# Performance work log

Measured on AMD Instinct MI355X. Metric: run time of the kernel, lower is better.

The kernel has to match this reference:

```python
import jax, jax.numpy as jnp
import numpy as np

INTERP = 10  # gt contour interpolation factor (time=10 in source)
SMOOTH_L1_BETA = 1.0
LOSS_WEIGHT = 1.0


def interpolation(poly):
    # poly: [B, M, 2] -> [B, M*INTERP, 2]
    poly_roll = jnp.roll(poly, shift=1, axis=1)
    step = jnp.arange(INTERP, dtype=poly.dtype) / INTERP  # [INTERP]
    # [B, M, INTERP, 2]
    interp = (poly[:, :, None, :] * step[None, None, :, None]
              + poly_roll[:, :, None, :] * (1.0 - step)[None, None, :, None])
    B, M = poly.shape[0], poly.shape[1]
    return interp.reshape(B, M * INTERP, 2)


def compute_distance(pred, gt):
    # pred: [B, N, 2], gt: [B, M, 2] -> squared euclidean distance [B, M, N]
    # ||g - p||^2 = ||g||^2 + ||p||^2 - 2 g.p  (avoids materializing [B,M,N,2])
    g2 = jnp.sum(gt * gt, axis=-1)[:, :, None]    # [B, M, 1]
    p2 = jnp.sum(pred * pred, axis=-1)[:, None, :]  # [B, 1, N]
    gp = jnp.einsum('bmk,bnk->bmn', gt, pred)
    return g2 + p2 - 2.0 * gp


def smooth_l1(x, y):
    d = jnp.abs(x - y)
    return jnp.where(d < SMOOTH_L1_BETA, 0.5 * d * d / SMOOTH_L1_BETA, d - 0.5 * SMOOTH_L1_BETA)


def setup_inputs() -> dict:
    key = jax.random.key(0)
    k1, k2, k3, k4 = jax.random.split(key, 4)
    B, N, M = 1024, 128, 128
    ini_pred_poly = jax.random.normal(k1, (B, N, 2), dtype=jnp.float32)
    pred_poly = ini_pred_poly + 0.1 * jax.random.normal(k2, (B, N, 2), dtype=jnp.float32)
    gt_poly = jax.random.normal(k3, (B, M, 2), dtype=jnp.float32)
    keyPointsMask = (jax.random.uniform(k4, (B, M)) < 0.7).astype(jnp.float32)
    return {'ini_pred_poly': ini_pred_poly, 'pred_poly': pred_poly,
            'gt_poly': gt_poly, 'keyPointsMask': keyPointsMask}


def reference(ini_pred_poly, pred_poly, gt_poly, keyPointsMask):
    # --- lossPred2NearestGt ---
    gt_interp = interpolation(gt_poly)                       # [B, M*10, 2]
    d1 = compute_distance(ini_pred_poly, gt_interp)          # [B, M*10, N]
    index_gt = jnp.argmin(d1, axis=1)                        # [B, N]
    nearest_gt = jnp.take_along_axis(gt_interp, index_gt[:, :, None], axis=1)  # [B, N, 2]
    loss_pred2gt = jnp.mean(smooth_l1(pred_poly, nearest_gt))  # scalar (reduction='mean')

    # --- lossGt2NearestPred ---
    d2 = compute_distance(ini_pred_poly, gt_poly)            # [B, M, N]
    index_pred = jnp.argmin(d2, axis=2)                      # [B, M]
    nearest_pred = jnp.take_along_axis(pred_poly, index_pred[:, :, None], axis=1)  # [B, M, 2]
    loss_gt2pred = smooth_l1(nearest_pred, gt_poly)          # [B, M, 2] (reduction='none')

    # mask expanded to [B, M, 2] in the source -> its sum counts both coords
    mask = keyPointsMask[:, :, None]
    masked_sum = jnp.sum(loss_gt2pred * mask)
    mask_sum = 2.0 * jnp.sum(keyPointsMask)
    loss_set2set = masked_sum / (mask_sum + 1.0) + loss_pred2gt
    loss = loss_set2set / 2.0
    return LOSS_WEIGHT * loss
```

## Files before the change

kernel.cpp:

```cpp
#include <hip/hip_runtime.h>
#include <math.h>


#define BB 1024
#define NN 128
#define MM 128

__device__ __forceinline__ float sl1(float x) {
    float d = fabsf(x);
    return d < 1.0f ? 0.5f * d * d : d - 0.5f;
}

__global__ void __launch_bounds__(512, 4)
dmloss_main(const float* __restrict__ ini, const float* __restrict__ pred,
            const float* __restrict__ gt,  const float* __restrict__ kmask,
            float4* __restrict__ partials)
{
    const int b   = blockIdx.x;
    const int tid = threadIdx.x;
    const int g   = tid & 63;
    const int h   = tid >> 6;

    __shared__ __align__(16) float2 s_gt[MM];
    __shared__ float2 s_pr[NN];
    __shared__ float2 s_ii[NN];
    __shared__ float4 s_segA[MM];
    __shared__ float2 s_segB[MM];
    __shared__ float  s_step[16];
    __shared__ float  s_rv[8 * 128];
    __shared__ float  s_rf[8 * 128];
    __shared__ float  s_sum[3][8];

    const float2* gt2 = (const float2*)(gt   + (size_t)b * MM * 2);
    const float2* in2 = (const float2*)(ini  + (size_t)b * NN * 2);
    const float2* pr2 = (const float2*)(pred + (size_t)b * NN * 2);

    float2 myPr = make_float2(0.f, 0.f);
    float  myKm = 0.f;
    if (tid < 128) {
        int m = tid;
        float2 gm = gt2[m];
        float2 a  = gt2[(m + 127) & 127];
        s_gt[m] = gm;
        float ex = gm.x - a.x, ey = gm.y - a.y;
        float A  = ex * ex + ey * ey;
        float inv = A > 0.f ? 10.f / A : 0.f;
        s_segA[m] = make_float4(a.x, a.y, -ex * inv, -ey * inv);
        s_segB[m] = make_float2(ex * 0.1f, ey * 0.1f);
        myPr = pr2[m];
        myKm = kmask[b * MM + m];
    } else if (tid < 256) {
        s_pr[tid - 128] = pr2[tid - 128];
    } else if (tid < 384) {
        s_ii[tid - 256] = in2[tid - 256];
    } else if (tid < 400) {
        s_step[tid - 384] = (float)(tid - 384) / 10.0f;
    }

    float4 pv = *(const float4*)(&in2[2 * g]);
    const float px0 = pv.x, py0 = pv.y, px1 = pv.z, py1 = pv.w;
    __syncthreads();

    float sumA = 0.f, sumB = 0.f, sumC = 0.f;

    float b0 = INFINITY, b1 = INFINITY;
    float f0 = 1e30f, f1 = 1e30f;
    {
        float fm = (float)(160 * h);
        const int m0 = 16 * h;
        #pragma unroll 2
        for (int j = 0; j < 16; ++j) {
            float4 SA = s_segA[m0 + j];
            float2 SB = s_segB[m0 + j];
            const float ax = SA.x, ay = SA.y, Xn = SA.z, Yn = SA.w;
            const float ux = SB.x, uy = SB.y;
            {
                float qx = ax - px0, qy = ay - py0;
                float jv = fmaf(qy, Yn, qx * Xn);
                float jr = rintf(__builtin_amdgcn_fmed3f(jv, 0.f, 9.f));
                float dx = fmaf(jr, ux, qx);
                float dy = fmaf(jr, uy, qy);
                float d  = fmaf(dy, dy, dx * dx);
                float fi = fm + jr;
                if (d < b0) { b0 = d; f0 = fi; }
            }
            {
                float qx = ax - px1, qy = ay - py1;
                float jv = fmaf(qy, Yn, qx * Xn);
                float jr = rintf(__builtin_amdgcn_fmed3f(jv, 0.f, 9.f));
                float dx = fmaf(jr, ux, qx);
                float dy = fmaf(jr, uy, qy);
                float d  = fmaf(dy, dy, dx * dx);
                float fi = fm + jr;
                if (d < b1) { b1 = d; f1 = fi; }
            }
            fm += 10.f;
        }
    }
    {
        float2* rv2 = (float2*)&s_rv[h * 128 + 2 * g];
        float2* rf2 = (float2*)&s_rf[h * 128 + 2 * g];
        *rv2 = make_float2(b0, b1);
        *rf2 = make_float2(f0, f1);
    }
    __syncthreads();

    if (tid < 128) {
        float best = s_rv[tid], bf = s_rf[tid];
        #pragma unroll
        for (int q = 1; q < 8; ++q) {
            float ov = s_rv[q * 128 + tid];
            float of = s_rf[q * 128 + tid];
            if (ov < best || (ov == best && of < bf)) { best = ov; bf = of; }
        }
        int bidx = (int)bf;
        int m = bidx / 10;
        int j = bidx - m * 10;
        float s  = s_step[j];
        float tt = 1.0f - s;
        float2 gm = s_gt[m];
        float2 gp = s_gt[(m + 127) & 127];
        float gx = gm.x * s + gp.x * tt;
        float gy = gm.y * s + gp.y * tt;
        sumA = sl1(myPr.x - gx) + sl1(myPr.y - gy);
    }
    __syncthreads();

    {
        float4 gv = *(const float4*)(&s_gt[2 * g]);
        const float gx0 = gv.x, gy0 = gv.y, gx1 = gv.z, gy1 = gv.w;
        b0 = INFINITY; b1 = INFINITY;
        f0 = 1e30f; f1 = 1e30f;
        float fk = (float)(16 * h);
        const int k0 = 16 * h;
        #pragma unroll 4
        for (int j = 0; j < 16; ++j) {
            float2 I = s_ii[k0 + j];
            {
                float dx = I.x - gx0, dy = I.y - gy0;
                float d  = fmaf(dy, dy, dx * dx);
                if (d < b0) { b0 = d; f0 = fk; }
            }
            {
                float dx = I.x - gx1, dy = I.y - gy1;
                float d  = fmaf(dy, dy, dx * dx);
                if (d < b1) { b1 = d; f1 = fk; }
            }
            fk += 1.f;
        }
        float2* rv2 = (float2*)&s_rv[h * 128 + 2 * g];
        float2* rf2 = (float2*)&s_rf[h * 128 + 2 * g];
        *rv2 = make_float2(b0, b1);
        *rf2 = make_float2(f0, f1);
    }
    __syncthreads();

    if (tid < 128) {
        float best = s_rv[tid], bf = s_rf[tid];
        #pragma unroll
        for (int q = 1; q < 8; ++q) {
            float ov = s_rv[q * 128 + tid];
            float of = s_rf[q * 128 + tid];
            if (ov < best || (ov == best && of < bf)) { best = ov; bf = of; }
        }
        int k = (int)bf;
        float2 pk2 = s_pr[k];
        float2 g0  = s_gt[tid];
        sumB = myKm * (sl1(pk2.x - g0.x) + sl1(pk2.y - g0.y));
        sumC = myKm;
    }

    #pragma unroll
    for (int off = 32; off > 0; off >>= 1) {
        sumA += __shfl_down(sumA, off);
        sumB += __shfl_down(sumB, off);
        sumC += __shfl_down(sumC, off);
    }
    const int wave = tid >> 6;
    if ((tid & 63) == 0) {
        s_sum[0][wave] = sumA; s_sum[1][wave] = sumB; s_sum[2][wave] = sumC;
    }
    __syncthreads();
    if (tid == 0) {
        float A = 0.f, Bs = 0.f, C = 0.f;
        #pragma unroll
        for (int w = 0; w < 8; ++w) {
            A += s_sum[0][w]; Bs += s_sum[1][w]; C += s_sum[2][w];
        }
        partials[b] = make_float4(A, Bs, C, 0.0f);
    }
}

__global__ void __launch_bounds__(256)
dmloss_final(const float4* __restrict__ partials, float* __restrict__ out)
{
    const int tid = threadIdx.x;
    float A = 0.0f, Bs = 0.0f, C = 0.0f;
    #pragma unroll
    for (int i = tid; i < BB; i += 256) {
        float4 p = partials[i];
        A += p.x; Bs += p.y; C += p.z;
    }
    #pragma unroll
    for (int off = 32; off > 0; off >>= 1) {
        A  += __shfl_down(A, off);
        Bs += __shfl_down(Bs, off);
        C  += __shfl_down(C, off);
    }
    __shared__ float sA[4], sB[4], sC[4];
    const int wave = tid >> 6, lane = tid & 63;
    if (lane == 0) { sA[wave] = A; sB[wave] = Bs; sC[wave] = C; }
    __syncthreads();
    if (tid == 0) {
        float a  = sA[0] + sA[1] + sA[2] + sA[3];
        float bs = sB[0] + sB[1] + sB[2] + sB[3];
        float c  = sC[0] + sC[1] + sC[2] + sC[3];
        float loss_pred2gt = a / ((float)BB * (float)NN * 2.0f);
        float loss_set2set = bs / (2.0f * c + 1.0f) + loss_pred2gt;
        out[0] = 0.5f * loss_set2set;
    }
}

extern "C" void kernel_launch(void* const* d_in, const int* in_sizes, int n_in,
                              void* d_out, int out_size, void* d_ws, size_t ws_size,
                              hipStream_t stream)
{
    const float* ini   = (const float*)d_in[0];
    const float* pred  = (const float*)d_in[1];
    const float* gt    = (const float*)d_in[2];
    const float* kmask = (const float*)d_in[3];
    float4* partials = (float4*)d_ws;

    dmloss_main<<<dim3(BB), dim3(512), 0, stream>>>(ini, pred, gt, kmask, partials);
    dmloss_final<<<dim3(1), dim3(256), 0, stream>>>(partials, (float*)d_out);
}
```

Before: 19.08 us.

## Split pred2gt and gt2pred phases into separate blocks per batch

Measured after the change: 20.33 us. 1.07x slower.

```diff
diff --git a/kernel.cpp b/kernel.cpp
--- a/kernel.cpp
+++ b/kernel.cpp
@@ -12,21 +12,22 @@
 }
 
 __global__ void __launch_bounds__(512, 4)
-dmloss_main(const float* __restrict__ ini, const float* __restrict__ pred,
-            const float* __restrict__ gt,  const float* __restrict__ kmask,
-            float4* __restrict__ partials)
+dmloss_phase(const float* __restrict__ ini, const float* __restrict__ pred,
+             const float* __restrict__ gt,  const float* __restrict__ kmask,
+             float* __restrict__ pA, float2* __restrict__ pBC)
 {
-    const int b   = blockIdx.x;
+    const int bid = blockIdx.x;
+    const int b   = bid >> 1;
     const int tid = threadIdx.x;
     const int g   = tid & 63;
     const int h   = tid >> 6;
 
     __shared__ __align__(16) float2 s_gt[MM];
-    __shared__ float2 s_pr[NN];
-    __shared__ float2 s_ii[NN];
     __shared__ float4 s_segA[MM];
     __shared__ float2 s_segB[MM];
     __shared__ float  s_step[16];
+    __shared__ float2 s_pr[NN];
+    __shared__ float2 s_ii[NN];
     __shared__ float  s_rv[8 * 128];
     __shared__ float  s_rf[8 * 128];
     __shared__ float  s_sum[3][8];
@@ -34,172 +35,174 @@
     const float2* gt2 = (const float2*)(gt   + (size_t)b * MM * 2);
     const float2* in2 = (const float2*)(ini  + (size_t)b * NN * 2);
     const float2* pr2 = (const float2*)(pred + (size_t)b * NN * 2);
-
-    float2 myPr = make_float2(0.f, 0.f);
-    float  myKm = 0.f;
-    if (tid < 128) {
-        int m = tid;
-        float2 gm = gt2[m];
-        float2 a  = gt2[(m + 127) & 127];
-        s_gt[m] = gm;
-        float ex = gm.x - a.x, ey = gm.y - a.y;
-        float A  = ex * ex + ey * ey;
-        float inv = A > 0.f ? 10.f / A : 0.f;
-        s_segA[m] = make_float4(a.x, a.y, -ex * inv, -ey * inv);
-        s_segB[m] = make_float2(ex * 0.1f, ey * 0.1f);
-        myPr = pr2[m];
-        myKm = kmask[b * MM + m];
-    } else if (tid < 256) {
-        s_pr[tid - 128] = pr2[tid - 128];
-    } else if (tid < 384) {
-        s_ii[tid - 256] = in2[tid - 256];
-    } else if (tid < 400) {
-        s_step[tid - 384] = (float)(tid - 384) / 10.0f;
-    }
-
-    float4 pv = *(const float4*)(&in2[2 * g]);
-    const float px0 = pv.x, py0 = pv.y, px1 = pv.z, py1 = pv.w;
-    __syncthreads();
-
-    float sumA = 0.f, sumB = 0.f, sumC = 0.f;
-
-    float b0 = INFINITY, b1 = INFINITY;
-    float f0 = 1e30f, f1 = 1e30f;
-    {
-        float fm = (float)(160 * h);
-        const int m0 = 16 * h;
-        #pragma unroll 2
-        for (int j = 0; j < 16; ++j) {
-            float4 SA = s_segA[m0 + j];
-            float2 SB = s_segB[m0 + j];
-            const float ax = SA.x, ay = SA.y, Xn = SA.z, Yn = SA.w;
-            const float ux = SB.x, uy = SB.y;
-            {
-                float qx = ax - px0, qy = ay - py0;
-                float jv = fmaf(qy, Yn, qx * Xn);
-                float jr = rintf(__builtin_amdgcn_fmed3f(jv, 0.f, 9.f));
-                float dx = fmaf(jr, ux, qx);
-                float dy = fmaf(jr, uy, qy);
-                float d  = fmaf(dy, dy, dx * dx);
-                float fi = fm + jr;
-                if (d < b0) { b0 = d; f0 = fi; }
-            }
-            {
-                float qx = ax - px1, qy = ay - py1;
-                float jv = fmaf(qy, Yn, qx * Xn);
-                float jr = rintf(__builtin_amdgcn_fmed3f(jv, 0.f, 9.f));
-                float dx = fmaf(jr, ux, qx);
-                float dy = fmaf(jr, uy, qy);
-                float d  = fmaf(dy, dy, dx * dx);
-                float fi = fm + jr;
-                if (d < b1) { b1 = d; f1 = fi; }
-            }
-            fm += 10.f;
-        }
-    }
-    {
-        float2* rv2 = (float2*)&s_rv[h * 128 + 2 * g];
-        float2* rf2 = (float2*)&s_rf[h * 128 + 2 * g];
-        *rv2 = make_float2(b0, b1);
-        *rf2 = make_float2(f0, f1);
-    }
-    __syncthreads();
-
-    if (tid < 128) {
-        float best = s_rv[tid], bf = s_rf[tid];
+    const int wave = tid >> 6;
+
+    if ((bid & 1) == 0) {
+        float2 myPr = make_float2(0.f, 0.f);
+        if (tid < 128) {
+            int m = tid;
+            float2 gm = gt2[m];
+            float2 a  = gt2[(m + 127) & 127];
+            s_gt[m] = gm;
+            float ex = gm.x - a.x, ey = gm.y - a.y;
+            float A  = ex * ex + ey * ey;
+            float inv = A > 0.f ? 10.f / A : 0.f;
+            s_segA[m] = make_float4(a.x, a.y, -ex * inv, -ey * inv);
+            s_segB[m] = make_float2(ex * 0.1f, ey * 0.1f);
+            myPr = pr2[m];
+        } else if (tid < 144) {
+            s_step[tid - 128] = (float)(tid - 128) / 10.0f;
+        }
+        float4 pv = *(const float4*)(&in2[2 * g]);
+        const float px0 = pv.x, py0 = pv.y, px1 = pv.z, py1 = pv.w;
+        __syncthreads();
+
+        float b0 = INFINITY, b1 = INFINITY;
+        float f0 = 1e30f, f1 = 1e30f;
+        {
+            float fm = (float)(160 * h);
+            const int m0 = 16 * h;
+            #pragma unroll 2
+            for (int j = 0; j < 16; ++j) {
+                float4 SA = s_segA[m0 + j];
+                float2 SB = s_segB[m0 + j];
+                const float ax = SA.x, ay = SA.y, Xn = SA.z, Yn = SA.w;
+                const float ux = SB.x, uy = SB.y;
+                {
+                    float qx = ax - px0, qy = ay - py0;
+                    float jv = fmaf(qy, Yn, qx * Xn);
+                    float jr = rintf(__builtin_amdgcn_fmed3f(jv, 0.f, 9.f));
+                    float dx = fmaf(jr, ux, qx);
+                    float dy = fmaf(jr, uy, qy);
+                    float d  = fmaf(dy, dy, dx * dx);
+                    float fi = fm + jr;
+                    if (d < b0) { b0 = d; f0 = fi; }
+                }
+                {
+                    float qx = ax - px1, qy = ay - py1;
+                    float jv = fmaf(qy, Yn, qx * Xn);
+                    float jr = rintf(__builtin_amdgcn_fmed3f(jv, 0.f, 9.f));
+                    float dx = fmaf(jr, ux, qx);
+                    float dy = fmaf(jr, uy, qy);
+                    float d  = fmaf(dy, dy, dx * dx);
+                    float fi = fm + jr;
+                    if (d < b1) { b1 = d; f1 = fi; }
+                }
+                fm += 10.f;
+            }
+        }
+        *(float2*)&s_rv[h * 128 + 2 * g] = make_float2(b0, b1);
+        *(float2*)&s_rf[h * 128 + 2 * g] = make_float2(f0, f1);
+        __syncthreads();
+
+        float sumA = 0.f;
+        if (tid < 128) {
+            float best = s_rv[tid], bf = s_rf[tid];
+            #pragma unroll
+            for (int q = 1; q < 8; ++q) {
+                float ov = s_rv[q * 128 + tid];
+                float of = s_rf[q * 128 + tid];
+                if (ov < best || (ov == best && of < bf)) { best = ov; bf = of; }
+            }
+            int bidx = (int)bf;
+            int m = bidx / 10;
+            int j = bidx - m * 10;
+            float s  = s_step[j];
+            float tt = 1.0f - s;
+            float2 gm = s_gt[m];
+            float2 gp = s_gt[(m + 127) & 127];
+            float gx = gm.x * s + gp.x * tt;
+            float gy = gm.y * s + gp.y * tt;
+            sumA = sl1(myPr.x - gx) + sl1(myPr.y - gy);
+        }
         #pragma unroll
-        for (int q = 1; q < 8; ++q) {
-            float ov = s_rv[q * 128 + tid];
-            float of = s_rf[q * 128 + tid];
-            if (ov < best || (ov == best && of < bf)) { best = ov; bf = of; }
-        }
-        int bidx = (int)bf;
-        int m = bidx / 10;
-        int j = bidx - m * 10;
-        float s  = s_step[j];
-        float tt = 1.0f - s;
-        float2 gm = s_gt[m];
-        float2 gp = s_gt[(m + 127) & 127];
-        float gx = gm.x * s + gp.x * tt;
-        float gy = gm.y * s + gp.y * tt;
-        sumA = sl1(myPr.x - gx) + sl1(myPr.y - gy);
-    }
-    __syncthreads();
-
-    {
-        float4 gv = *(const float4*)(&s_gt[2 * g]);
+        for (int off = 32; off > 0; off >>= 1) sumA += __shfl_down(sumA, off);
+        if ((tid & 63) == 0) s_sum[0][wave] = sumA;
+        __syncthreads();
+        if (tid == 0) {
+            float A = 0.f;
+            #pragma unroll
+            for (int w = 0; w < 8; ++w) A += s_sum[0][w];
+            pA[b] = A;
+        }
+    } else {
+        float myKm = 0.f;
+        if (tid < 128) {
+            s_ii[tid] = in2[tid];
+            s_pr[tid] = pr2[tid];
+            myKm = kmask[b * MM + tid];
+        }
+        float4 gv = *(const float4*)(&gt2[2 * g]);
         const float gx0 = gv.x, gy0 = gv.y, gx1 = gv.z, gy1 = gv.w;
-        b0 = INFINITY; b1 = INFINITY;
-        f0 = 1e30f; f1 = 1e30f;
-        float fk = (float)(16 * h);
-        const int k0 = 16 * h;
-        #pragma unroll 4
-        for (int j = 0; j < 16; ++j) {
-            float2 I = s_ii[k0 + j];
-            {
-                float dx = I.x - gx0, dy = I.y - gy0;
-                float d  = fmaf(dy, dy, dx * dx);
-                if (d < b0) { b0 = d; f0 = fk; }
-            }
-            {
-                float dx = I.x - gx1, dy = I.y - gy1;
-                float d  = fmaf(dy, dy, dx * dx);
-                if (d < b1) { b1 = d; f1 = fk; }
-            }
-            fk += 1.f;
-        }
-        float2* rv2 = (float2*)&s_rv[h * 128 + 2 * g];
-        float2* rf2 = (float2*)&s_rf[h * 128 + 2 * g];
-        *rv2 = make_float2(b0, b1);
-        *rf2 = make_float2(f0, f1);
-    }
-    __syncthreads();
-
-    if (tid < 128) {
-        float best = s_rv[tid], bf = s_rf[tid];
+        __syncthreads();
+
+        float b0 = INFINITY, b1 = INFINITY;
+        float f0 = 1e30f, f1 = 1e30f;
+        {
+            float fk = (float)(16 * h);
+            const int k0 = 16 * h;
+            #pragma unroll 4
+            for (int j = 0; j < 16; ++j) {
+                float2 I = s_ii[k0 + j];
+                {
+                    float dx = I.x - gx0, dy = I.y - gy0;
+                    float d  = fmaf(dy, dy, dx * dx);
+                    if (d < b0) { b0 = d; f0 = fk; }
+                }
+                {
+                    float dx = I.x - gx1, dy = I.y - gy1;
+                    float d  = fmaf(dy, dy, dx * dx);
+                    if (d < b1) { b1 = d; f1 = fk; }
+                }
+                fk += 1.f;
+            }
+        }
+        *(float2*)&s_rv[h * 128 + 2 * g] = make_float2(b0, b1);
+        *(float2*)&s_rf[h * 128 + 2 * g] = make_float2(f0, f1);
+        __syncthreads();
+
+        float sumB = 0.f, sumC = 0.f;
+        if (tid < 128) {
+            float best = s_rv[tid], bf = s_rf[tid];
+            #pragma unroll
+            for (int q = 1; q < 8; ++q) {
+                float ov = s_rv[q * 128 + tid];
+                float of = s_rf[q * 128 + tid];
+                if (ov < best || (ov == best && of < bf)) { best = ov; bf = of; }
+            }
+            int k = (int)bf;
+            float2 pk2 = s_pr[k];
+            float2 g0  = gt2[tid];
+            sumB = myKm * (sl1(pk2.x - g0.x) + sl1(pk2.y - g0.y));
+            sumC = myKm;
+        }
         #pragma unroll
-        for (int q = 1; q < 8; ++q) {
-            float ov = s_rv[q * 128 + tid];
-            float of = s_rf[q * 128 + tid];
-            if (ov < best || (ov == best && of < bf)) { best = ov; bf = of; }
-        }
-        int k = (int)bf;
-        float2 pk2 = s_pr[k];
-        float2 g0  = s_gt[tid];
-        sumB = myKm * (sl1(pk2.x - g0.x) + sl1(pk2.y - g0.y));
-        sumC = myKm;
-    }
-
-    #pragma unroll
-    for (int off = 32; off > 0; off >>= 1) {
-        sumA += __shfl_down(sumA, off);
-        sumB += __shfl_down(sumB, off);
-        sumC += __shfl_down(sumC, off);
-    }
-    const int wave = tid >> 6;
-    if ((tid & 63) == 0) {
-        s_sum[0][wave] = sumA; s_sum[1][wave] = sumB; s_sum[2][wave] = sumC;
-    }
-    __syncthreads();
-    if (tid == 0) {
-        float A = 0.f, Bs = 0.f, C = 0.f;
-        #pragma unroll
-        for (int w = 0; w < 8; ++w) {
-            A += s_sum[0][w]; Bs += s_sum[1][w]; C += s_sum[2][w];
-        }
-        partials[b] = make_float4(A, Bs, C, 0.0f);
+        for (int off = 32; off > 0; off >>= 1) {
+            sumB += __shfl_down(sumB, off);
+            sumC += __shfl_down(sumC, off);
+        }
+        if ((tid & 63) == 0) { s_sum[1][wave] = sumB; s_sum[2][wave] = sumC; }
+        __syncthreads();
+        if (tid == 0) {
+            float Bs = 0.f, C = 0.f;
+            #pragma unroll
+            for (int w = 0; w < 8; ++w) { Bs += s_sum[1][w]; C += s_sum[2][w]; }
+            pBC[b] = make_float2(Bs, C);
+        }
     }
 }
 
 __global__ void __launch_bounds__(256)
-dmloss_final(const float4* __restrict__ partials, float* __restrict__ out)
+dmloss_final(const float* __restrict__ pA, const float2* __restrict__ pBC,
+             float* __restrict__ out)
 {
     const int tid = threadIdx.x;
     float A = 0.0f, Bs = 0.0f, C = 0.0f;
     #pragma unroll
     for (int i = tid; i < BB; i += 256) {
-        float4 p = partials[i];
-        A += p.x; Bs += p.y; C += p.z;
+        A += pA[i];
+        float2 p = pBC[i];
+        Bs += p.x; C += p.y;
     }
     #pragma unroll
     for (int off = 32; off > 0; off >>= 1) {
@@ -229,8 +232,11 @@
     const float* pred  = (const float*)d_in[1];
     const float* gt    = (const float*)d_in[2];
     const float* kmask = (const float*)d_in[3];
-    float4* partials = (float4*)d_ws;
-
-    dmloss_main<<<dim3(BB), dim3(512), 0, stream>>>(ini, pred, gt, kmask, partials);
-    dmloss_final<<<dim3(1), dim3(256), 0, stream>>>(partials, (float*)d_out);
-}
+
+    float*  pA  = (float*)d_ws;
+    float2* pBC = (float2*)(pA + BB);
+
+    dmloss_phase<<<dim3(2 * BB), dim3(512), 0, stream>>>(ini, pred, gt, kmask,
+                                                         pA, pBC);
+    dmloss_final<<<dim3(1), dim3(256), 0, stream>>>(pA, pBC, (float*)d_out);
+}
```

## Split each batch across two 256-thread blocks, one point per thread

Applied to the files above, without the earlier changes.

After: 18.08 us. 1.06x faster.

```diff
diff --git a/kernel.cpp b/kernel.cpp
--- a/kernel.cpp
+++ b/kernel.cpp
@@ -11,15 +11,17 @@
     return d < 1.0f ? 0.5f * d * d : d - 0.5f;
 }
 
-__global__ void __launch_bounds__(512, 4)
+__global__ void __launch_bounds__(256, 8)
 dmloss_main(const float* __restrict__ ini, const float* __restrict__ pred,
             const float* __restrict__ gt,  const float* __restrict__ kmask,
             float4* __restrict__ partials)
 {
-    const int b   = blockIdx.x;
-    const int tid = threadIdx.x;
-    const int g   = tid & 63;
-    const int h   = tid >> 6;
+    const int b    = blockIdx.x >> 1;
+    const int half = blockIdx.x & 1;
+    const int tid  = threadIdx.x;
+    const int g    = tid & 63;
+    const int h    = tid >> 6;
+    const int P    = (half << 6) + g;
 
     __shared__ __align__(16) float2 s_gt[MM];
     __shared__ float2 s_pr[NN];
@@ -27,16 +29,14 @@
     __shared__ float4 s_segA[MM];
     __shared__ float2 s_segB[MM];
     __shared__ float  s_step[16];
-    __shared__ float  s_rv[8 * 128];
-    __shared__ float  s_rf[8 * 128];
-    __shared__ float  s_sum[3][8];
+    __shared__ float  s_rv[4 * 64];
+    __shared__ float  s_rf[4 * 64];
+    __shared__ float  s_sum[3][4];
 
     const float2* gt2 = (const float2*)(gt   + (size_t)b * MM * 2);
     const float2* in2 = (const float2*)(ini  + (size_t)b * NN * 2);
     const float2* pr2 = (const float2*)(pred + (size_t)b * NN * 2);
 
-    float2 myPr = make_float2(0.f, 0.f);
-    float  myKm = 0.f;
     if (tid < 128) {
         int m = tid;
         float2 gm = gt2[m];
@@ -47,70 +47,50 @@
         float inv = A > 0.f ? 10.f / A : 0.f;
         s_segA[m] = make_float4(a.x, a.y, -ex * inv, -ey * inv);
         s_segB[m] = make_float2(ex * 0.1f, ey * 0.1f);
-        myPr = pr2[m];
-        myKm = kmask[b * MM + m];
-    } else if (tid < 256) {
-        s_pr[tid - 128] = pr2[tid - 128];
-    } else if (tid < 384) {
-        s_ii[tid - 256] = in2[tid - 256];
-    } else if (tid < 400) {
-        s_step[tid - 384] = (float)(tid - 384) / 10.0f;
-    }
-
-    float4 pv = *(const float4*)(&in2[2 * g]);
-    const float px0 = pv.x, py0 = pv.y, px1 = pv.z, py1 = pv.w;
+        if (tid < 16) s_step[tid] = (float)tid / 10.0f;
+    } else {
+        int k = tid - 128;
+        s_pr[k] = pr2[k];
+        s_ii[k] = in2[k];
+    }
+    float2 myP  = in2[P];
+    float2 myPr = pr2[P];
+    float2 myG  = gt2[P];
+    float  myKm = kmask[b * MM + P];
+    const float px = myP.x, py = myP.y;
     __syncthreads();
 
     float sumA = 0.f, sumB = 0.f, sumC = 0.f;
 
-    float b0 = INFINITY, b1 = INFINITY;
-    float f0 = 1e30f, f1 = 1e30f;
+    float b0 = INFINITY, f0 = 1e30f;
     {
-        float fm = (float)(160 * h);
-        const int m0 = 16 * h;
-        #pragma unroll 2
-        for (int j = 0; j < 16; ++j) {
+        float fm = (float)(320 * h);
+        const int m0 = 32 * h;
+        #pragma unroll 4
+        for (int j = 0; j < 32; ++j) {
             float4 SA = s_segA[m0 + j];
             float2 SB = s_segB[m0 + j];
-            const float ax = SA.x, ay = SA.y, Xn = SA.z, Yn = SA.w;
-            const float ux = SB.x, uy = SB.y;
-            {
-                float qx = ax - px0, qy = ay - py0;
-                float jv = fmaf(qy, Yn, qx * Xn);
-                float jr = rintf(__builtin_amdgcn_fmed3f(jv, 0.f, 9.f));
-                float dx = fmaf(jr, ux, qx);
-                float dy = fmaf(jr, uy, qy);
-                float d  = fmaf(dy, dy, dx * dx);
-                float fi = fm + jr;
-                if (d < b0) { b0 = d; f0 = fi; }
-            }
-            {
-                float qx = ax - px1, qy = ay - py1;
-                float jv = fmaf(qy, Yn, qx * Xn);
-                float jr = rintf(__builtin_amdgcn_fmed3f(jv, 0.f, 9.f));
-                float dx = fmaf(jr, ux, qx);
-                float dy = fmaf(jr, uy, qy);
-                float d  = fmaf(dy, dy, dx * dx);
-                float fi = fm + jr;
-                if (d < b1) { b1 = d; f1 = fi; }
-            }
+            float qx = SA.x - px, qy = SA.y - py;
+            float jv = fmaf(qy, SA.w, qx * SA.z);
+            float jr = rintf(__builtin_amdgcn_fmed3f(jv, 0.f, 9.f));
+            float dx = fmaf(jr, SB.x, qx);
+            float dy = fmaf(jr, SB.y, qy);
+            float d  = fmaf(dy, dy, dx * dx);
+            float fi = fm + jr;
+            if (d < b0) { b0 = d; f0 = fi; }
             fm += 10.f;
         }
     }
-    {
-        float2* rv2 = (float2*)&s_rv[h * 128 + 2 * g];
-        float2* rf2 = (float2*)&s_rf[h * 128 + 2 * g];
-        *rv2 = make_float2(b0, b1);
-        *rf2 = make_float2(f0, f1);
-    }
-    __syncthreads();
-
-    if (tid < 128) {
+    s_rv[h * 64 + g] = b0;
+    s_rf[h * 64 + g] = f0;
+    __syncthreads();
+
+    if (tid < 64) {
         float best = s_rv[tid], bf = s_rf[tid];
         #pragma unroll
-        for (int q = 1; q < 8; ++q) {
-            float ov = s_rv[q * 128 + tid];
-            float of = s_rf[q * 128 + tid];
+        for (int q = 1; q < 4; ++q) {
+            float ov = s_rv[q * 64 + tid];
+            float of = s_rf[q * 64 + tid];
             if (ov < best || (ov == best && of < bf)) { best = ov; bf = of; }
         }
         int bidx = (int)bf;
@@ -122,52 +102,43 @@
         float2 gp = s_gt[(m + 127) & 127];
         float gx = gm.x * s + gp.x * tt;
         float gy = gm.y * s + gp.y * tt;
-        sumA = sl1(myPr.x - gx) + sl1(myPr.y - gy);
+        float2 pr = s_pr[(half << 6) + tid];
+        sumA = sl1(pr.x - gx) + sl1(pr.y - gy);
     }
     __syncthreads();
 
     {
-        float4 gv = *(const float4*)(&s_gt[2 * g]);
-        const float gx0 = gv.x, gy0 = gv.y, gx1 = gv.z, gy1 = gv.w;
-        b0 = INFINITY; b1 = INFINITY;
-        f0 = 1e30f; f1 = 1e30f;
-        float fk = (float)(16 * h);
-        const int k0 = 16 * h;
+        const float gx = myG.x, gy = myG.y;
+        b0 = INFINITY; f0 = 1e30f;
+        float fk = (float)(32 * h);
+        const int k0 = 32 * h;
         #pragma unroll 4
-        for (int j = 0; j < 16; ++j) {
+        for (int j = 0; j < 32; ++j) {
             float2 I = s_ii[k0 + j];
-            {
-                float dx = I.x - gx0, dy = I.y - gy0;
-                float d  = fmaf(dy, dy, dx * dx);
-                if (d < b0) { b0 = d; f0 = fk; }
-            }
-            {
-                float dx = I.x - gx1, dy = I.y - gy1;
-                float d  = fmaf(dy, dy, dx * dx);
-                if (d < b1) { b1 = d; f1 = fk; }
-            }
+            float dx = I.x - gx, dy = I.y - gy;
+            float d  = fmaf(dy, dy, dx * dx);
+            if (d < b0) { b0 = d; f0 = fk; }
             fk += 1.f;
         }
-        float2* rv2 = (float2*)&s_rv[h * 128 + 2 * g];
-        float2* rf2 = (float2*)&s_rf[h * 128 + 2 * g];
-        *rv2 = make_float2(b0, b1);
-        *rf2 = make_float2(f0, f1);
-    }
-    __syncthreads();
-
-    if (tid < 128) {
+        s_rv[h * 64 + g] = b0;
+        s_rf[h * 64 + g] = f0;
+    }
+    __syncthreads();
+
+    if (tid < 64) {
         float best = s_rv[tid], bf = s_rf[tid];
         #pragma unroll
-        for (int q = 1; q < 8; ++q) {
-            float ov = s_rv[q * 128 + tid];
-            float of = s_rf[q * 128 + tid];
+        for (int q = 1; q < 4; ++q) {
+            float ov = s_rv[q * 64 + tid];
+            float of = s_rf[q * 64 + tid];
             if (ov < best || (ov == best && of < bf)) { best = ov; bf = of; }
         }
         int k = (int)bf;
         float2 pk2 = s_pr[k];
-        float2 g0  = s_gt[tid];
-        sumB = myKm * (sl1(pk2.x - g0.x) + sl1(pk2.y - g0.y));
-        sumC = myKm;
+        float2 g0  = s_gt[(half << 6) + tid];
+        float  km  = kmask[b * MM + (half << 6) + tid];
+        sumB = km * (sl1(pk2.x - g0.x) + sl1(pk2.y - g0.y));
+        sumC = km;
     }
 
     #pragma unroll
@@ -184,10 +155,10 @@
     if (tid == 0) {
         float A = 0.f, Bs = 0.f, C = 0.f;
         #pragma unroll
-        for (int w = 0; w < 8; ++w) {
+        for (int w = 0; w < 4; ++w) {
             A += s_sum[0][w]; Bs += s_sum[1][w]; C += s_sum[2][w];
         }
-        partials[b] = make_float4(A, Bs, C, 0.0f);
+        partials[blockIdx.x] = make_float4(A, Bs, C, 0.0f);
     }
 }
 
@@ -197,7 +168,7 @@
     const int tid = threadIdx.x;
     float A = 0.0f, Bs = 0.0f, C = 0.0f;
     #pragma unroll
-    for (int i = tid; i < BB; i += 256) {
+    for (int i = tid; i < 2 * BB; i += 256) {
         float4 p = partials[i];
         A += p.x; Bs += p.y; C += p.z;
     }
@@ -231,6 +202,6 @@
     const float* kmask = (const float*)d_in[3];
     float4* partials = (float4*)d_ws;
 
-    dmloss_main<<<dim3(BB), dim3(512), 0, stream>>>(ini, pred, gt, kmask, partials);
+    dmloss_main<<<dim3(2 * BB), dim3(256), 0, stream>>>(ini, pred, gt, kmask, partials);
     dmloss_final<<<dim3(1), dim3(256), 0, stream>>>(partials, (float*)d_out);
 }
```
